# Kernel optimization log

Measured on AMD Instinct MI355X. Metric: run time of the kernel, lower is better.

The kernel has to match this reference:

```python
import jax, jax.numpy as jnp
import numpy as np

L, D, H, N, R = 4, 256, 512, 16, 8  # layers, d_model, hidden=2*d_model, state_dim, dt_rank
OUT_LEN, IN_DIM = 96, 32
EPS = 1e-5


def _layernorm(v, g, b):
    m = jnp.mean(v, axis=-1, keepdims=True)
    var = jnp.mean((v - m) ** 2, axis=-1, keepdims=True)
    return (v - m) / jnp.sqrt(var + EPS) * g + b


def _pos_encoding(T, d):
    pos = jnp.arange(T, dtype=jnp.float32)[:, None]
    div = jnp.exp(jnp.arange(0, d, 2, dtype=jnp.float32) * (-np.log(10000.0) / d))
    pe = jnp.zeros((T, d), dtype=jnp.float32)
    pe = pe.at[:, 0::2].set(jnp.sin(pos * div))
    pe = pe.at[:, 1::2].set(jnp.cos(pos * div))
    return pe


def setup_inputs() -> dict:
    key = jax.random.key(0)
    ks = jax.random.split(key, 20)
    inp = {
        "x": jax.random.normal(ks[0], (8, 1024, IN_DIM), dtype=jnp.float32),
        "emb_w": jax.random.normal(ks[1], (D, IN_DIM), dtype=jnp.float32) * 0.1,
        "emb_b": jnp.zeros((D,), dtype=jnp.float32),
        "norm_g": jnp.ones((L, D), dtype=jnp.float32),
        "norm_b": jnp.zeros((L, D), dtype=jnp.float32),
        "in_w": jax.random.normal(ks[2], (L, H, D), dtype=jnp.float32) * (1.0 / np.sqrt(D)),
        "conv_w": jax.random.normal(ks[3], (L, H, 1, 3), dtype=jnp.float32) * 0.5,
        "A_p": jax.random.normal(ks[4], (L, H, N), dtype=jnp.float32) * 0.01,
        "D_p": jnp.ones((L, H), dtype=jnp.float32),
        "dt1_w": jax.random.normal(ks[5], (L, R, H), dtype=jnp.float32) * (1.0 / np.sqrt(H)),
        "dt1_b": jnp.zeros((L, R), dtype=jnp.float32),
        "dt2_w": jax.random.normal(ks[6], (L, H, R), dtype=jnp.float32) * (1.0 / np.sqrt(R)),
        "dt2_b": jnp.zeros((L, H), dtype=jnp.float32),
        "out_w": jax.random.normal(ks[7], (L, D, H), dtype=jnp.float32) * (1.0 / np.sqrt(H)),
        "final_g": jnp.ones((D,), dtype=jnp.float32),
        "final_b": jnp.zeros((D,), dtype=jnp.float32),
        "head1_w": jax.random.normal(ks[8], (D, D), dtype=jnp.float32) * (1.0 / np.sqrt(D)),
        "head1_b": jnp.zeros((D,), dtype=jnp.float32),
        "head2_w": jax.random.normal(ks[9], (OUT_LEN, D), dtype=jnp.float32) * (1.0 / np.sqrt(D)),
        "head2_b": jnp.zeros((OUT_LEN,), dtype=jnp.float32),
    }
    return inp


def _mamba_block(h, g, b, in_w, conv_w, A_p, D_p, dt1_w, dt1_b, dt2_w, dt2_b, out_w):
    res = h
    v = _layernorm(h, g, b)            # [B,T,D]
    v = jnp.einsum('btd,hd->bth', v, in_w)  # [B,T,H]
    # depthwise conv1d, kernel 3, padding 1, groups=H
    vc = jnp.transpose(v, (0, 2, 1))   # [B,H,T]
    vc = jax.lax.conv_general_dilated(vc, conv_w, window_strides=(1,),
                                      padding=[(1, 1)], feature_group_count=H,
                                      dimension_numbers=('NCH', 'OIH', 'NCH'))
    v = jnp.transpose(jax.nn.silu(vc), (0, 2, 1))  # [B,T,H]
    dt = jax.nn.relu(jnp.einsum('bth,rh->btr', v, dt1_w) + dt1_b)
    dt = jnp.einsum('btr,hr->bth', dt, dt2_w) + dt2_b
    dt = jax.nn.softplus(dt)           # [B,T,H]
    A = -jnp.exp(A_p)                  # [H,N]
    safe_A = jnp.where(jnp.abs(A) < 1e-5, jnp.ones_like(A), A)

    B_sz = v.shape[0]
    state0 = jnp.zeros((B_sz, H, N), dtype=v.dtype)

    def step(state, inp):
        x_t, dt_t = inp  # [B,H] each
        dA = A * dt_t[..., None]            # [B,H,N]
        discA = jnp.exp(dA)
        discB = (discA - 1.0) / safe_A * dt_t[..., None]
        state = discA * state + discB * x_t[..., None]
        y = jnp.einsum('bhn,hn->bh', state, A_p) + D_p * x_t
        return state, y

    xs = (jnp.transpose(v, (1, 0, 2)), jnp.transpose(dt, (1, 0, 2)))  # [T,B,H]
    _, ys = jax.lax.scan(step, state0, xs)
    y = jnp.transpose(ys, (1, 0, 2))   # [B,T,H]
    return res + jnp.einsum('bth,dh->btd', y, out_w)


def reference(x, emb_w, emb_b, norm_g, norm_b, in_w, conv_w, A_p, D_p,
              dt1_w, dt1_b, dt2_w, dt2_b, out_w, final_g, final_b,
              head1_w, head1_b, head2_w, head2_b):
    h = jnp.einsum('bti,di->btd', x, emb_w) + emb_b  # [B,T,D]
    h = h + _pos_encoding(h.shape[1], D)[None]
    for l in range(L):
        h = _mamba_block(h, norm_g[l], norm_b[l], in_w[l], conv_w[l], A_p[l],
                         D_p[l], dt1_w[l], dt1_b[l], dt2_w[l], dt2_b[l], out_w[l])
    h = _layernorm(h, final_g, final_b)
    h = h[:, -1, :]                    # last token [B,D]
    h = jax.nn.silu(h @ head1_w.T + head1_b)
    return h @ head2_w.T + head2_b     # [B, OUT_LEN]
```

## Files before the change

kernel.cpp:

```cpp
#include <hip/hip_runtime.h>
#include <hip/hip_bf16.h>
#include <math.h>

#define BB 8
#define TT 1024
#define DD 256
#define HH 512
#define NN 16
#define RR 8
#define OUT_LEN 96
#define IN_DIM 32
#define MM (BB*TT)

#define SC 16
#define CC (TT/SC)

typedef unsigned short u16;
typedef unsigned int u32;
typedef __attribute__((ext_vector_type(8))) short short8;
typedef __attribute__((ext_vector_type(8))) unsigned short u16x8;
typedef __attribute__((ext_vector_type(4))) float float4v;

__device__ __forceinline__ u16 f2bf(float f) {
    __hip_bfloat16 h = __float2bfloat16(f);
    return *(u16*)&h;
}
__device__ __forceinline__ float bf2f(u16 u) {
    u32 v = ((u32)u) << 16;
    return *(float*)&v;
}

#define GLD_LDS16(src, dst) __builtin_amdgcn_global_load_lds( \
    (const __attribute__((address_space(1))) void*)(src),     \
    (__attribute__((address_space(3))) void*)(dst), 16, 0, 0)

__global__ __launch_bounds__(256) void embed_ln_kernel(
    const float* __restrict__ x, const float* __restrict__ emb_w,
    const float* __restrict__ emb_b,
    const float* __restrict__ g, const float* __restrict__ b,
    float* __restrict__ h, u16* __restrict__ lnout)
{
    int bt = blockIdx.x;
    int d  = threadIdx.x;
    int t  = bt & (TT - 1);

    __shared__ float xs[IN_DIM];
    __shared__ float red[4], red2[4];
    if (threadIdx.x < IN_DIM) xs[threadIdx.x] = x[bt * IN_DIM + threadIdx.x];
    __syncthreads();

    const float* w = emb_w + d * IN_DIM;
    float acc = emb_b[d];
#pragma unroll
    for (int i = 0; i < IN_DIM; i++) acc = fmaf(xs[i], w[i], acc);

    int i2 = d & ~1;
    float div = expf(-(float)i2 * (logf(10000.0f) / (float)DD));
    float arg = (float)t * div;
    float pe = (d & 1) ? cosf(arg) : sinf(arg);
    float val = acc + pe;
    h[bt * DD + d] = val;

    float s = val;
#pragma unroll
    for (int o = 32; o > 0; o >>= 1) s += __shfl_down(s, o);
    int lane = d & 63, wave = d >> 6;
    if (lane == 0) red[wave] = s;
    __syncthreads();
    float mean = (red[0] + red[1] + red[2] + red[3]) * (1.0f / DD);

    float c = val - mean;
    float s2 = c * c;
#pragma unroll
    for (int o = 32; o > 0; o >>= 1) s2 += __shfl_down(s2, o);
    if (lane == 0) red2[wave] = s2;
    __syncthreads();
    float var = (red2[0] + red2[1] + red2[2] + red2[3]) * (1.0f / DD);

    lnout[bt * DD + d] = f2bf(c * rsqrtf(var + 1e-5f) * g[d] + b[d]);
}

__global__ __launch_bounds__(256) void cvt_bf16_kernel(
    const float* __restrict__ in1, u16* __restrict__ out1, int n1,
    const float* __restrict__ in2, u16* __restrict__ out2, int n2)
{
    int i = blockIdx.x * 256 + threadIdx.x;
    if (i < n1) out1[i] = f2bf(in1[i]);
    else if (i < n1 + n2) out2[i - n1] = f2bf(in2[i - n1]);
}

__global__ __launch_bounds__(256) void ln_kernel(
    const float* __restrict__ h, const float* __restrict__ g,
    const float* __restrict__ b, u16* __restrict__ out)
{
    int bt = blockIdx.x;
    int d  = threadIdx.x;
    float v = h[bt * DD + d];

    __shared__ float red[4], red2[4];
    float s = v;
#pragma unroll
    for (int o = 32; o > 0; o >>= 1) s += __shfl_down(s, o);
    int lane = d & 63, wave = d >> 6;
    if (lane == 0) red[wave] = s;
    __syncthreads();
    float mean = (red[0] + red[1] + red[2] + red[3]) * (1.0f / DD);

    float c = v - mean;
    float s2 = c * c;
#pragma unroll
    for (int o = 32; o > 0; o >>= 1) s2 += __shfl_down(s2, o);
    if (lane == 0) red2[wave] = s2;
    __syncthreads();
    float var = (red2[0] + red2[1] + red2[2] + red2[3]) * (1.0f / DD);

    out[bt * DD + d] = f2bf(c * rsqrtf(var + 1e-5f) * g[d] + b[d]);
}

template<int BM, int BN, int OUT_BF16>
__global__ __launch_bounds__(256) void gemm_bf16(
    const u16* __restrict__ A, const u16* __restrict__ B,
    void* __restrict__ Cv, int M, int N, int K, int addC)
{
    constexpr int BK = 64;
    constexpr int MT = BM / 32;
    constexpr int NT = BN / 32;
    static_assert(BN == 64, "B staging assumes BN==64");

    __shared__ __align__(16) u16 Al[8][BM][8];
    __shared__ __align__(16) u16 Bl[8][BN][8];

    const int tid = threadIdx.x;
    const int bm = blockIdx.y * BM;
    const int bn = blockIdx.x * BN;
    const int wid = tid >> 6, lane = tid & 63;
    const int wm = wid >> 1, wn = wid & 1;
    const int lq = lane >> 4, lm = lane & 15;

    float4v acc[MT][NT];
#pragma unroll
    for (int i = 0; i < MT; i++)
#pragma unroll
        for (int j = 0; j < NT; j++) acc[i][j] = (float4v){0.f, 0.f, 0.f, 0.f};

    for (int k0 = 0; k0 < K; k0 += BK) {
#pragma unroll
        for (int it = 0; it < (8 * BM) / 256; it++) {
            int c = it * 256 + tid;
            int q = c / BM, row = c % BM;
            GLD_LDS16(A + (size_t)(bm + row) * K + k0 + q * 8, &Al[q][row][0]);
        }
#pragma unroll
        for (int it = 0; it < (8 * BN) / 256; it++) {
            int c = it * 256 + tid;
            int q = c / BN, row = c % BN;
            GLD_LDS16(B + (size_t)(bn + row) * K + k0 + q * 8, &Bl[q][row][0]);
        }
        __syncthreads();

        short8 af[2][MT], bf[2][NT];
#pragma unroll
        for (int kk = 0; kk < 2; kk++) {
#pragma unroll
            for (int mt = 0; mt < MT; mt++)
                af[kk][mt] = *(const short8*)&Al[kk * 4 + lq][wm * (BM / 2) + mt * 16 + lm][0];
#pragma unroll
            for (int nt = 0; nt < NT; nt++)
                bf[kk][nt] = *(const short8*)&Bl[kk * 4 + lq][wn * (BN / 2) + nt * 16 + lm][0];
        }

#pragma unroll
        for (int kk = 0; kk < 2; kk++)
#pragma unroll
            for (int mt = 0; mt < MT; mt++)
#pragma unroll
                for (int nt = 0; nt < NT; nt++)
                    acc[mt][nt] = __builtin_amdgcn_mfma_f32_16x16x32_bf16(
                        af[kk][mt], bf[kk][nt], acc[mt][nt], 0, 0, 0);
        __syncthreads();
    }

#pragma unroll
    for (int mt = 0; mt < MT; mt++)
#pragma unroll
        for (int nt = 0; nt < NT; nt++) {
            int row0 = bm + wm * (BM / 2) + mt * 16 + lq * 4;
            int col  = bn + wn * (BN / 2) + nt * 16 + lm;
#pragma unroll
            for (int r = 0; r < 4; r++) {
                float vv = acc[mt][nt][r];
                if (OUT_BF16) {
                    ((u16*)Cv)[(size_t)(row0 + r) * N + col] = f2bf(vv);
                } else {
                    float* cp = (float*)Cv + (size_t)(row0 + r) * N + col;
                    if (addC) vv += *cp;
                    *cp = vv;
                }
            }
        }
}

__global__ __launch_bounds__(256) void conv_dt1_kernel(
    const u16* __restrict__ v,
    const float* __restrict__ cwg,
    const float* __restrict__ w1g,
    const float* __restrict__ b1g,
    u16* __restrict__ vsb,
    float* __restrict__ dtr)
{
    __shared__ float w1s[RR * 2 * 256];
    int tid = threadIdx.x;
    {
        int lane = tid & 63, rc = tid >> 6;
#pragma unroll
        for (int i = 0; i < 4; i++) {
            int rci = rc + i * 4;
            int r = rci >> 1, jc = rci & 1;
            float4 wv = *(const float4*)(w1g + r * HH + lane * 8 + jc * 4);
            *(float4*)&w1s[rci * 256 + lane * 4] = wv;
        }
    }
    __syncthreads();

    int wave = tid >> 6, lane = tid & 63;
    int m = blockIdx.x * 4 + wave;
    int t = m & (TT - 1);
    int h0 = lane * 8;

    const u16* vrow = v + (size_t)m * HH + h0;
    u16x8 x0 = *(const u16x8*)vrow;
    u16x8 xm = (t > 0)      ? *(const u16x8*)(vrow - HH) : (u16x8)(0);
    u16x8 xp = (t < TT - 1) ? *(const u16x8*)(vrow + HH) : (u16x8)(0);

    const float* wp = cwg + h0 * 3;
    float a[8];
    u16x8 o;
#pragma unroll
    for (int j = 0; j < 8; j++) {
        float s = wp[j * 3] * bf2f(xm[j]);
        s = fmaf(wp[j * 3 + 1], bf2f(x0[j]), s);
        s = fmaf(wp[j * 3 + 2], bf2f(xp[j]), s);
        s = s / (1.0f + __expf(-s));
        a[j] = s;
        o[j] = f2bf(s);
    }
    *(u16x8*)(vsb + (size_t)m * HH + h0) = o;

    float acc[RR];
#pragma unroll
    for (int r = 0; r < RR; r++) {
        float4 wlo = *(const float4*)&w1s[(r * 2 + 0) * 256 + lane * 4];
        float4 whi = *(const float4*)&w1s[(r * 2 + 1) * 256 + lane * 4];
        float s = a[0] * wlo.x;
        s = fmaf(a[1], wlo.y, s);
        s = fmaf(a[2], wlo.z, s);
        s = fmaf(a[3], wlo.w, s);
        s = fmaf(a[4], whi.x, s);
        s = fmaf(a[5], whi.y, s);
        s = fmaf(a[6], whi.z, s);
        s = fmaf(a[7], whi.w, s);
        acc[r] = s;
    }
#pragma unroll
    for (int r = 0; r < RR; r++) {
#pragma unroll
        for (int o2 = 1; o2 < 64; o2 <<= 1) acc[r] += __shfl_xor(acc[r], o2);
    }
    if (lane == 0) {
#pragma unroll
        for (int r = 0; r < RR; r++) acc[r] = fmaxf(acc[r] + b1g[r], 0.0f);
        *(float4*)(dtr + (size_t)m * RR)     = make_float4(acc[0], acc[1], acc[2], acc[3]);
        *(float4*)(dtr + (size_t)m * RR + 4) = make_float4(acc[4], acc[5], acc[6], acc[7]);
    }
}

__device__ __forceinline__ float softplus_f(float s) {
    return (s > 20.0f) ? s : __logf(1.0f + __expf(s));
}

__global__ __launch_bounds__(256) void scan_pass1(
    const u16* __restrict__ vs,
    const float* __restrict__ dtr,
    const float* __restrict__ dt2_w,
    const float* __restrict__ dt2_b,
    const float* __restrict__ A_p,
    float* __restrict__ Lst,
    float* __restrict__ sdt)
{
    int h = blockIdx.x * 256 + threadIdx.x;
    int c = blockIdx.y;
    int b = blockIdx.z;

    float A[NN], invA[NN], st[NN];
    const float* ap = A_p + h * NN;
#pragma unroll
    for (int n = 0; n < NN; n++) {
        float a = -__expf(ap[n]);
        A[n] = a; invA[n] = 1.0f / a; st[n] = 0.0f;
    }
    float w2[RR];
#pragma unroll
    for (int r = 0; r < RR; r++) w2[r] = dt2_w[h * RR + r];
    float b2 = dt2_b[h];

    const u16*   vbase = vs  + ((size_t)b * TT + (size_t)c * SC) * HH + h;
    const float* drow  = dtr + ((size_t)b * TT + (size_t)c * SC) * RR;

    float dr[RR];
#pragma unroll
    for (int r = 0; r < RR; r++) dr[r] = drow[r];

    float s_dt = 0.0f;
#pragma unroll 2
    for (int t = 0; t < SC; t++) {
        float drn[RR];
        if (t + 1 < SC) {
#pragma unroll
            for (int r = 0; r < RR; r++) drn[r] = drow[(t + 1) * RR + r];
        }
        float s = b2;
#pragma unroll
        for (int r = 0; r < RR; r++) s = fmaf(dr[r], w2[r], s);
        float dt = softplus_f(s);
        float xv = bf2f(vbase[(size_t)t * HH]);
        s_dt += dt;
#pragma unroll
        for (int n = 0; n < NN; n++) {
            float e  = __expf(A[n] * dt);
            float dB = (e - 1.0f) * invA[n] * dt;
            st[n] = fmaf(e, st[n], dB * xv);
        }
#pragma unroll
        for (int r = 0; r < RR; r++) dr[r] = drn[r];
    }

    size_t base = (((size_t)c * BB + b) * HH + h) * NN;
#pragma unroll
    for (int n = 0; n < NN; n += 4)
        *(float4*)(Lst + base + n) = make_float4(st[n], st[n+1], st[n+2], st[n+3]);
    sdt[((size_t)c * BB + b) * HH + h] = s_dt;
}

__global__ __launch_bounds__(256) void scan_carry(
    const float* __restrict__ A_p, const float* __restrict__ sdt,
    float* __restrict__ Lst)
{
    int i = blockIdx.x * 256 + threadIdx.x;
    int n  = i & (NN - 1);
    int bh = i >> 4;
    int h  = bh & (HH - 1);
    int b  = bh >> 9;

    float A = -__expf(A_p[h * NN + n]);
    float E = 0.0f;
    for (int c = 0; c < CC; c++) {
        size_t sidx = ((size_t)c * BB + b) * HH + h;
        float P = __expf(A * sdt[sidx]);
        size_t lidx = sidx * NN + n;
        float Lc = Lst[lidx];
        Lst[lidx] = E;
        E = fmaf(P, E, Lc);
    }
}

__global__ __launch_bounds__(256) void scan_pass2(
    const u16* __restrict__ vs,
    const float* __restrict__ dtr,
    const float* __restrict__ dt2_w,
    const float* __restrict__ dt2_b,
    const float* __restrict__ A_p, const float* __restrict__ D_p,
    const float* __restrict__ carry,
    u16* __restrict__ y)
{
    int h = blockIdx.x * 256 + threadIdx.x;
    int c = blockIdx.y;
    int b = blockIdx.z;

    float A[NN], invA[NN], Ap[NN], st[NN];
    const float* app = A_p + h * NN;
    size_t cbase = (((size_t)c * BB + b) * HH + h) * NN;
#pragma unroll
    for (int n = 0; n < NN; n += 4) {
        float4 c4 = *(const float4*)(carry + cbase + n);
        st[n] = c4.x; st[n+1] = c4.y; st[n+2] = c4.z; st[n+3] = c4.w;
    }
#pragma unroll
    for (int n = 0; n < NN; n++) {
        float apv = app[n];
        Ap[n] = apv;
        float a = -__expf(apv);
        A[n] = a; invA[n] = 1.0f / a;
    }
    float w2[RR];
#pragma unroll
    for (int r = 0; r < RR; r++) w2[r] = dt2_w[h * RR + r];
    float b2 = dt2_b[h];
    float Dp = D_p[h];

    const u16*   vbase = vs  + ((size_t)b * TT + (size_t)c * SC) * HH + h;
    const float* drow  = dtr + ((size_t)b * TT + (size_t)c * SC) * RR;
    u16*         ybase = y   + ((size_t)b * TT + (size_t)c * SC) * HH + h;

    float dr[RR];
#pragma unroll
    for (int r = 0; r < RR; r++) dr[r] = drow[r];

#pragma unroll 2
    for (int t = 0; t < SC; t++) {
        float drn[RR];
        if (t + 1 < SC) {
#pragma unroll
            for (int r = 0; r < RR; r++) drn[r] = drow[(t + 1) * RR + r];
        }
        float s = b2;
#pragma unroll
        for (int r = 0; r < RR; r++) s = fmaf(dr[r], w2[r], s);
        float dt = softplus_f(s);
        float xv = bf2f(vbase[(size_t)t * HH]);
        float acc = Dp * xv;
#pragma unroll
        for (int n = 0; n < NN; n++) {
            float e  = __expf(A[n] * dt);
            float dB = (e - 1.0f) * invA[n] * dt;
            st[n] = fmaf(e, st[n], dB * xv);
            acc = fmaf(st[n], Ap[n], acc);
        }
        ybase[(size_t)t * HH] = f2bf(acc);
#pragma unroll
        for (int r = 0; r < RR; r++) dr[r] = drn[r];
    }
}

__global__ __launch_bounds__(256) void head_kernel(
    const float* __restrict__ h,
    const float* __restrict__ fg, const float* __restrict__ fb,
    const float* __restrict__ w1, const float* __restrict__ b1,
    const float* __restrict__ w2, const float* __restrict__ b2,
    float* __restrict__ out)
{
    int b = blockIdx.x;
    int d = threadIdx.x;
    __shared__ float hn[DD], s1[DD];
    __shared__ float red[4];

    float v = h[((size_t)b * TT + (TT - 1)) * DD + d];

    float s = v;
#pragma unroll
    for (int o = 32; o > 0; o >>= 1) s += __shfl_down(s, o);
    int lane = d & 63, wave = d >> 6;
    if (lane == 0) red[wave] = s;
    __syncthreads();
    float mean = (red[0] + red[1] + red[2] + red[3]) * (1.0f / DD);
    __syncthreads();

    float c = v - mean;
    float s2 = c * c;
#pragma unroll
    for (int o = 32; o > 0; o >>= 1) s2 += __shfl_down(s2, o);
    if (lane == 0) red[wave] = s2;
    __syncthreads();
    float var = (red[0] + red[1] + red[2] + red[3]) * (1.0f / DD);

    hn[d] = c * rsqrtf(var + 1e-5f) * fg[d] + fb[d];
    __syncthreads();

    float a1 = b1[d];
    const float* w1r = w1 + d * DD;
#pragma unroll 8
    for (int k = 0; k < DD; k++) a1 = fmaf(hn[k], w1r[k], a1);
    s1[d] = a1 / (1.0f + __expf(-a1));
    __syncthreads();

    if (d < OUT_LEN) {
        float a2 = b2[d];
        const float* w2r = w2 + d * DD;
#pragma unroll 8
        for (int k = 0; k < DD; k++) a2 = fmaf(s1[k], w2r[k], a2);
        out[b * OUT_LEN + d] = a2;
    }
}

extern "C" void kernel_launch(void* const* d_in, const int* in_sizes, int n_in,
                              void* d_out, int out_size, void* d_ws, size_t ws_size,
                              hipStream_t stream)
{
    (void)in_sizes; (void)n_in; (void)out_size; (void)ws_size;

    const float* x       = (const float*)d_in[0];
    const float* emb_w   = (const float*)d_in[1];
    const float* emb_b   = (const float*)d_in[2];
    const float* norm_g  = (const float*)d_in[3];
    const float* norm_b  = (const float*)d_in[4];
    const float* in_w    = (const float*)d_in[5];
    const float* conv_w  = (const float*)d_in[6];
    const float* A_p     = (const float*)d_in[7];
    const float* D_p     = (const float*)d_in[8];
    const float* dt1_w   = (const float*)d_in[9];
    const float* dt1_b   = (const float*)d_in[10];
    const float* dt2_w   = (const float*)d_in[11];
    const float* dt2_b   = (const float*)d_in[12];
    const float* out_w   = (const float*)d_in[13];
    const float* final_g = (const float*)d_in[14];
    const float* final_b = (const float*)d_in[15];
    const float* head1_w = (const float*)d_in[16];
    const float* head1_b = (const float*)d_in[17];
    const float* head2_w = (const float*)d_in[18];
    const float* head2_b = (const float*)d_in[19];
    float* outp = (float*)d_out;

    char* ws = (char*)d_ws;
    float* h    = (float*)ws;                 ws += (size_t)MM * DD * 4;
    u16*   vbf  = (u16*)ws;                   ws += (size_t)MM * HH * 2;
    u16*   vsb  = (u16*)ws;                   ws += (size_t)MM * HH * 2;
    u16*   yb_u = (u16*)ws;                   ws += (size_t)MM * HH * 2;
    float* dtr  = (float*)ws;                 ws += (size_t)MM * RR * 4;
    float* Lst  = (float*)ws;                 ws += (size_t)CC * BB * HH * NN * 4;
    float* sdt  = (float*)ws;                 ws += (size_t)CC * BB * HH * 4;
    u16*   wbf_in  = (u16*)ws;                ws += (size_t)4 * HH * DD * 2;
    u16*   wbf_out = (u16*)ws;                ws += (size_t)4 * DD * HH * 2;

    const int NW = 4 * HH * DD;
    cvt_bf16_kernel<<<(2 * NW) / 256, 256, 0, stream>>>(in_w, wbf_in, NW, out_w, wbf_out, NW);

    embed_ln_kernel<<<MM, 256, 0, stream>>>(x, emb_w, emb_b, norm_g, norm_b, h, yb_u);

    for (int l = 0; l < 4; l++) {
        if (l > 0)
            ln_kernel<<<MM, 256, 0, stream>>>(h, norm_g + l * DD, norm_b + l * DD, yb_u);
        gemm_bf16<128, 64, 1><<<dim3(HH / 64, MM / 128), 256, 0, stream>>>(
            yb_u, wbf_in + (size_t)l * HH * DD, vbf, MM, HH, DD, 0);
        conv_dt1_kernel<<<MM / 4, 256, 0, stream>>>(
            vbf, conv_w + (size_t)l * HH * 3,
            dt1_w + (size_t)l * RR * HH, dt1_b + l * RR, vsb, dtr);

        scan_pass1<<<dim3(HH / 256, CC, BB), 256, 0, stream>>>(
            vsb, dtr, dt2_w + (size_t)l * HH * RR, dt2_b + l * HH,
            A_p + (size_t)l * HH * NN, Lst, sdt);
        scan_carry<<<(BB * HH * NN) / 256, 256, 0, stream>>>(
            A_p + (size_t)l * HH * NN, sdt, Lst);
        scan_pass2<<<dim3(HH / 256, CC, BB), 256, 0, stream>>>(
            vsb, dtr, dt2_w + (size_t)l * HH * RR, dt2_b + l * HH,
            A_p + (size_t)l * HH * NN, D_p + l * HH, Lst, yb_u);

        gemm_bf16<64, 64, 0><<<dim3(DD / 64, MM / 64), 256, 0, stream>>>(
            yb_u, wbf_out + (size_t)l * DD * HH, h, MM, DD, HH, 1);
    }

    head_kernel<<<BB, 256, 0, stream>>>(h, final_g, final_b,
                                        head1_w, head1_b, head2_w, head2_b, outp);
}
```

Measured before the change: 535.8 us.

## Fuse out-projection GEMM with residual add and next-layer LayerNorm

Replaces the separate out-projection GEMM and the per-layer LayerNorm kernel with one kernel. Each block computes a full 32-row by 256-column output tile, adds the residual, writes h, reduces the row statistics in-block, and emits the bf16 normalized input for the next layer. This removes one launch per layer and a full re-read of h. In exchange the GEMM tiles are narrower in M with a wide N (256 blocks). Variance now comes from E[x^2]-mean^2 in a single pass, which is slightly less numerically robust.

```diff
diff --git a/kernel.cpp b/kernel.cpp
--- a/kernel.cpp
+++ b/kernel.cpp
@@ -87,34 +87,6 @@
     int i = blockIdx.x * 256 + threadIdx.x;
     if (i < n1) out1[i] = f2bf(in1[i]);
     else if (i < n1 + n2) out2[i - n1] = f2bf(in2[i - n1]);
-}
-
-__global__ __launch_bounds__(256) void ln_kernel(
-    const float* __restrict__ h, const float* __restrict__ g,
-    const float* __restrict__ b, u16* __restrict__ out)
-{
-    int bt = blockIdx.x;
-    int d  = threadIdx.x;
-    float v = h[bt * DD + d];
-
-    __shared__ float red[4], red2[4];
-    float s = v;
-#pragma unroll
-    for (int o = 32; o > 0; o >>= 1) s += __shfl_down(s, o);
-    int lane = d & 63, wave = d >> 6;
-    if (lane == 0) red[wave] = s;
-    __syncthreads();
-    float mean = (red[0] + red[1] + red[2] + red[3]) * (1.0f / DD);
-
-    float c = v - mean;
-    float s2 = c * c;
-#pragma unroll
-    for (int o = 32; o > 0; o >>= 1) s2 += __shfl_down(s2, o);
-    if (lane == 0) red2[wave] = s2;
-    __syncthreads();
-    float var = (red2[0] + red2[1] + red2[2] + red2[3]) * (1.0f / DD);
-
-    out[bt * DD + d] = f2bf(c * rsqrtf(var + 1e-5f) * g[d] + b[d]);
 }
 
 template<int BM, int BN, int OUT_BF16>
@@ -200,13 +172,111 @@
         }
 }
 
+__global__ __launch_bounds__(256) void gemm2_ln(
+    const u16* __restrict__ A, const u16* __restrict__ B,
+    float* __restrict__ h,
+    const float* __restrict__ g, const float* __restrict__ bb,
+    u16* __restrict__ lnout, int doLN)
+{
+    constexpr int BM = 32;
+    __shared__ __align__(16) u16 Al[8][BM][8];
+    __shared__ __align__(16) u16 Bl[8][256][8];
+    __shared__ float rs[2][BM], qs[2][BM];
+
+    const int tid = threadIdx.x;
+    const int bm = blockIdx.x * BM;
+    const int wid = tid >> 6, lane = tid & 63;
+    const int wm = wid >> 1, wn = wid & 1;
+    const int lq = lane >> 4, lm = lane & 15;
+
+    float4v acc[8];
+#pragma unroll
+    for (int j = 0; j < 8; j++) acc[j] = (float4v){0.f, 0.f, 0.f, 0.f};
+
+    for (int k0 = 0; k0 < 512; k0 += 64) {
+        {
+            int q = tid >> 5, row = tid & 31;
+            GLD_LDS16(A + (size_t)(bm + row) * 512 + k0 + q * 8, &Al[q][row][0]);
+        }
+#pragma unroll
+        for (int it = 0; it < 8; it++) {
+            int c = it * 256 + tid;
+            int q = c >> 8, row = c & 255;
+            GLD_LDS16(B + (size_t)row * 512 + k0 + q * 8, &Bl[q][row][0]);
+        }
+        __syncthreads();
+
+        short8 af[2], bf[2][8];
+#pragma unroll
+        for (int kk = 0; kk < 2; kk++) {
+            af[kk] = *(const short8*)&Al[kk * 4 + lq][wm * 16 + lm][0];
+#pragma unroll
+            for (int nt = 0; nt < 8; nt++)
+                bf[kk][nt] = *(const short8*)&Bl[kk * 4 + lq][wn * 128 + nt * 16 + lm][0];
+        }
+#pragma unroll
+        for (int kk = 0; kk < 2; kk++)
+#pragma unroll
+            for (int nt = 0; nt < 8; nt++)
+                acc[nt] = __builtin_amdgcn_mfma_f32_16x16x32_bf16(
+                    af[kk], bf[kk][nt], acc[nt], 0, 0, 0);
+        __syncthreads();
+    }
+
+    float val[4][8];
+    float s1[4] = {0.f, 0.f, 0.f, 0.f}, s2[4] = {0.f, 0.f, 0.f, 0.f};
+#pragma unroll
+    for (int r = 0; r < 4; r++) {
+        int row = bm + wm * 16 + lq * 4 + r;
+#pragma unroll
+        for (int nt = 0; nt < 8; nt++) {
+            int col = wn * 128 + nt * 16 + lm;
+            float v = acc[nt][r] + h[(size_t)row * DD + col];
+            val[r][nt] = v;
+            s1[r] += v;
+            s2[r] = fmaf(v, v, s2[r]);
+            h[(size_t)row * DD + col] = v;
+        }
+    }
+#pragma unroll
+    for (int r = 0; r < 4; r++) {
+#pragma unroll
+        for (int o = 1; o < 16; o <<= 1) {
+            s1[r] += __shfl_xor(s1[r], o);
+            s2[r] += __shfl_xor(s2[r], o);
+        }
+    }
+    if (lm == 0) {
+#pragma unroll
+        for (int r = 0; r < 4; r++) {
+            rs[wn][wm * 16 + lq * 4 + r] = s1[r];
+            qs[wn][wm * 16 + lq * 4 + r] = s2[r];
+        }
+    }
+    __syncthreads();
+
+    if (doLN) {
+#pragma unroll
+        for (int r = 0; r < 4; r++) {
+            int i = wm * 16 + lq * 4 + r;
+            int row = bm + i;
+            float mean = (rs[0][i] + rs[1][i]) * (1.0f / DD);
+            float var  = (qs[0][i] + qs[1][i]) * (1.0f / DD) - mean * mean;
+            float rstd = rsqrtf(var + 1e-5f);
+#pragma unroll
+            for (int nt = 0; nt < 8; nt++) {
+                int col = wn * 128 + nt * 16 + lm;
+                lnout[(size_t)row * DD + col] =
+                    f2bf((val[r][nt] - mean) * rstd * g[col] + bb[col]);
+            }
+        }
+    }
+}
+
 __global__ __launch_bounds__(256) void conv_dt1_kernel(
-    const u16* __restrict__ v,
-    const float* __restrict__ cwg,
-    const float* __restrict__ w1g,
-    const float* __restrict__ b1g,
-    u16* __restrict__ vsb,
-    float* __restrict__ dtr)
+    const u16* __restrict__ v, const float* __restrict__ cwg,
+    const float* __restrict__ w1g, const float* __restrict__ b1g,
+    u16* __restrict__ vsb, float* __restrict__ dtr)
 {
     __shared__ float w1s[RR * 2 * 256];
     int tid = threadIdx.x;
@@ -279,13 +349,10 @@
 }
 
 __global__ __launch_bounds__(256) void scan_pass1(
-    const u16* __restrict__ vs,
-    const float* __restrict__ dtr,
-    const float* __restrict__ dt2_w,
-    const float* __restrict__ dt2_b,
+    const u16* __restrict__ vs, const float* __restrict__ dtr,
+    const float* __restrict__ dt2_w, const float* __restrict__ dt2_b,
     const float* __restrict__ A_p,
-    float* __restrict__ Lst,
-    float* __restrict__ sdt)
+    float* __restrict__ Lst, float* __restrict__ sdt)
 {
     int h = blockIdx.x * 256 + threadIdx.x;
     int c = blockIdx.y;
@@ -510,26 +577,25 @@
     float* outp = (float*)d_out;
 
     char* ws = (char*)d_ws;
-    float* h    = (float*)ws;                 ws += (size_t)MM * DD * 4;
-    u16*   vbf  = (u16*)ws;                   ws += (size_t)MM * HH * 2;
-    u16*   vsb  = (u16*)ws;                   ws += (size_t)MM * HH * 2;
-    u16*   yb_u = (u16*)ws;                   ws += (size_t)MM * HH * 2;
-    float* dtr  = (float*)ws;                 ws += (size_t)MM * RR * 4;
-    float* Lst  = (float*)ws;                 ws += (size_t)CC * BB * HH * NN * 4;
-    float* sdt  = (float*)ws;                 ws += (size_t)CC * BB * HH * 4;
+    float* h     = (float*)ws;                ws += (size_t)MM * DD * 4;
+    u16*   vbf   = (u16*)ws;                  ws += (size_t)MM * HH * 2;
+    u16*   vsb   = (u16*)ws;                  ws += (size_t)MM * HH * 2;
+    u16*   ybf   = (u16*)ws;                  ws += (size_t)MM * HH * 2;
+    u16*   lnbuf = (u16*)ws;                  ws += (size_t)MM * DD * 2;
+    float* dtr   = (float*)ws;                ws += (size_t)MM * RR * 4;
+    float* Lst   = (float*)ws;                ws += (size_t)CC * BB * HH * NN * 4;
+    float* sdt   = (float*)ws;                ws += (size_t)CC * BB * HH * 4;
     u16*   wbf_in  = (u16*)ws;                ws += (size_t)4 * HH * DD * 2;
     u16*   wbf_out = (u16*)ws;                ws += (size_t)4 * DD * HH * 2;
 
     const int NW = 4 * HH * DD;
     cvt_bf16_kernel<<<(2 * NW) / 256, 256, 0, stream>>>(in_w, wbf_in, NW, out_w, wbf_out, NW);
 
-    embed_ln_kernel<<<MM, 256, 0, stream>>>(x, emb_w, emb_b, norm_g, norm_b, h, yb_u);
+    embed_ln_kernel<<<MM, 256, 0, stream>>>(x, emb_w, emb_b, norm_g, norm_b, h, lnbuf);
 
     for (int l = 0; l < 4; l++) {
-        if (l > 0)
-            ln_kernel<<<MM, 256, 0, stream>>>(h, norm_g + l * DD, norm_b + l * DD, yb_u);
         gemm_bf16<128, 64, 1><<<dim3(HH / 64, MM / 128), 256, 0, stream>>>(
-            yb_u, wbf_in + (size_t)l * HH * DD, vbf, MM, HH, DD, 0);
+            lnbuf, wbf_in + (size_t)l * HH * DD, vbf, MM, HH, DD, 0);
         conv_dt1_kernel<<<MM / 4, 256, 0, stream>>>(
             vbf, conv_w + (size_t)l * HH * 3,
             dt1_w + (size_t)l * RR * HH, dt1_b + l * RR, vsb, dtr);
@@ -541,10 +607,13 @@
             A_p + (size_t)l * HH * NN, sdt, Lst);
         scan_pass2<<<dim3(HH / 256, CC, BB), 256, 0, stream>>>(
             vsb, dtr, dt2_w + (size_t)l * HH * RR, dt2_b + l * HH,
-            A_p + (size_t)l * HH * NN, D_p + l * HH, Lst, yb_u);
-
-        gemm_bf16<64, 64, 0><<<dim3(DD / 64, MM / 64), 256, 0, stream>>>(
-            yb_u, wbf_out + (size_t)l * DD * HH, h, MM, DD, HH, 1);
+            A_p + (size_t)l * HH * NN, D_p + l * HH, Lst, ybf);
+
+        const float* g_next = (l < 3) ? (norm_g + (l + 1) * DD) : final_g;
+        const float* b_next = (l < 3) ? (norm_b + (l + 1) * DD) : final_b;
+        gemm2_ln<<<MM / 32, 256, 0, stream>>>(
+            ybf, wbf_out + (size_t)l * DD * HH, h, g_next, b_next,
+            lnbuf, (l < 3) ? 1 : 0);
     }
 
     head_kernel<<<BB, 256, 0, stream>>>(h, final_g, final_b,
```

Measured after the change: 526.2 us. About the same (-1.8%).
